# Kernel optimization log

Measured on AMD Instinct MI355X. Metric: run time of the kernel, lower is better.

## Reference

```python
import jax, jax.numpy as jnp
import numpy as np


def setup_inputs() -> dict:
    B, S, DK, DV, H = 2, 2048, 1024, 1024, 16
    ks = jax.random.split(jax.random.key(0), 7)
    keys = jax.random.normal(ks[0], (B, S, DK), jnp.float32)
    queries = jax.random.normal(ks[1], (B, S, DK), jnp.float32)
    values = jax.random.normal(ks[2], (B, S, DV), jnp.float32)
    # per-head projection weights, stored as [H, in, out] (torch Linear uses W.T; math-equivalent)
    WQ = jax.random.normal(ks[3], (H, DK, DK // H), jnp.float32) / np.sqrt(DK).astype(np.float32)
    WK = jax.random.normal(ks[4], (H, DK, DK // H), jnp.float32) / np.sqrt(DK).astype(np.float32)
    WV = jax.random.normal(ks[5], (H, DV, DV // H), jnp.float32) / np.sqrt(DV).astype(np.float32)
    WO = jax.random.normal(ks[6], (DV, DV), jnp.float32) / np.sqrt(DV).astype(np.float32)
    return {"keys": keys, "queries": queries, "values": values,
            "WQ": WQ, "WK": WK, "WV": WV, "WO": WO, "masking": 1}


def reference(keys, queries, values, WQ, WK, WV, WO, masking):
    B, Sq, _ = queries.shape
    Sk = keys.shape[1]
    # batched per-head projections (original loops over heads in Python)
    Q = jnp.einsum('bqd,hde->bhqe', queries, WQ)   # [B,H,Sq,dh]
    K = jnp.einsum('bkd,hde->bhke', keys, WK)      # [B,H,Sk,dh]
    V = jnp.einsum('bkd,hde->bhke', values, WV)    # [B,H,Sk,dvh]
    q_idx = jnp.arange(Sq)[:, None]
    k_idx = jnp.arange(Sk)[None, :]
    causal = k_idx <= q_idx
    # NOTE: original never applies the slope m; bias = (i - j) for i<=j else 0, same for all heads
    bias = jnp.where(causal, (k_idx - q_idx).astype(jnp.float32), 0.0)
    scale = np.float32(1.0 / np.sqrt(Sk))  # original divides by sqrt(keys.shape[1])
    y = (jnp.einsum('bhqe,bhke->bhqk', Q, K) + bias) * scale
    if masking:
        y = jnp.where(causal, y, -jnp.inf)
    # original: F.softmax(y, 1) on [B,Sq,Sk] -> softmax over the QUERY axis
    z = jax.nn.softmax(y, axis=2)
    out = jnp.einsum('bhqk,bhke->bhqe', z, V)      # [B,H,Sq,dvh]
    out = out.transpose(0, 2, 1, 3).reshape(B, Sq, -1)  # concat heads on last dim
    return out @ WO
```

## Files before the change

### kernel.cpp

```cpp
#include <hip/hip_runtime.h>
#include <math.h>

#define SEQ    2048
#define DMODEL 1024
#define NH     16
#define DH     64
#define NB     2
#define BHN    (NB*NH)

static constexpr float SCALE = 0.02209708691207961f;

typedef __attribute__((ext_vector_type(8))) short short8;
typedef __attribute__((ext_vector_type(4))) short short4v;
typedef __attribute__((ext_vector_type(4))) float f32x4;

__device__ __forceinline__ short f2bf(float f) {
    union { float f; unsigned u; } v; v.f = f;
    unsigned r = (v.u + 0x7FFFu + ((v.u >> 16) & 1u)) >> 16;
    return (short)r;
}

__device__ __forceinline__ unsigned pack_bf2(float a, float b) {
    union { float f; unsigned u; } ua, ub; ua.f = a; ub.f = b;
    return __builtin_amdgcn_perm(ub.u + 0x8000u, ua.u + 0x8000u, 0x07060302u);
}

__device__ __forceinline__ float bf2f(short s) {
    union { unsigned u; float f; } v; v.u = ((unsigned)(unsigned short)s) << 16;
    return v.f;
}

__device__ __forceinline__ void load16_lds(const short* g, short* l) {
    __builtin_amdgcn_global_load_lds(
        (const __attribute__((address_space(1))) unsigned int*)g,
        (__attribute__((address_space(3))) unsigned int*)l,
        16, 0, 0);
}

__device__ __forceinline__ void stage_rows(const short* g, short* s, int t, int ldg, int nIter) {
    int wave = t >> 6, lane = t & 63;
    #pragma unroll
    for (int i = 0; i < 4; ++i) {
        if (i >= nIter) break;
        int E   = i * 2048 + wave * 512 + lane * 8;
        int row = E >> 6;
        int blk = (lane & 7) ^ (row & 7);
        load16_lds(g + (size_t)row * ldg + blk * 8, s + i * 2048 + wave * 512);
    }
}

__device__ __forceinline__ short8 frag_sw(const short* s, int rowbase, int ks, int lane) {
    int m   = rowbase + (lane & 15);
    int q   = lane >> 4;
    int blk = (ks * 4 + q) ^ (m & 7);
    return *(const short8*)(s + m * 64 + blk * 8);
}

__global__ __launch_bounds__(256) void convert_all(
    const float* __restrict__ q, const float* __restrict__ k, const float* __restrict__ v,
    short* __restrict__ Xq, short* __restrict__ Xk, short* __restrict__ Xv,
    const float* __restrict__ WQ, const float* __restrict__ WK,
    const float* __restrict__ WV, const float* __restrict__ WO,
    short* __restrict__ WQt, short* __restrict__ WKt,
    short* __restrict__ WVt, short* __restrict__ WOt)
{
    __shared__ float Ts[64][68];
    const int lin = blockIdx.x;
    const int t = threadIdx.x;

    if (lin < 6144) {
        const int z = lin / 2048, bx = lin - z * 2048;
        const float* src = (z == 0) ? q : (z == 1) ? k : v;
        short* dst = (z == 0) ? Xq : (z == 1) ? Xk : Xv;
        size_t idx = ((size_t)bx * 256 + t) * 8;
        float4 a = *(const float4*)(src + idx);
        float4 b = *(const float4*)(src + idx + 4);
        short8 o;
        o[0] = f2bf(a.x); o[1] = f2bf(a.y); o[2] = f2bf(a.z); o[3] = f2bf(a.w);
        o[4] = f2bf(b.x); o[5] = f2bf(b.y); o[6] = f2bf(b.z); o[7] = f2bf(b.w);
        *(short8*)(dst + idx) = o;
        return;
    }

    const int wl = lin - 6144;
    const int z = wl >> 8, rem = wl & 255;
    const int k0 = (rem & 15) * 64;
    const int ny = rem >> 4;
    const float* W = (z == 0) ? WQ : (z == 1) ? WK : (z == 2) ? WV : WO;
    short* Wt = (z == 0) ? WQt : (z == 1) ? WKt : (z == 2) ? WVt : WOt;

    const int tr = t >> 4, tc4 = (t & 15) * 4;
    #pragma unroll
    for (int i = 0; i < 4; ++i) {
        int row = tr + i * 16;
        float4 v4;
        if (z < 3) v4 = *(const float4*)(W + (size_t)ny * DMODEL * DH + (size_t)(k0 + row) * DH + tc4);
        else       v4 = *(const float4*)(W + (size_t)(k0 + row) * DMODEL + ny * 64 + tc4);
        Ts[tc4 + 0][row] = v4.x; Ts[tc4 + 1][row] = v4.y;
        Ts[tc4 + 2][row] = v4.z; Ts[tc4 + 3][row] = v4.w;
    }
    __syncthreads();
    #pragma unroll
    for (int i = 0; i < 4; ++i) {
        int nl = tr + i * 16;
        short4v o;
        o[0] = f2bf(Ts[nl][tc4 + 0]); o[1] = f2bf(Ts[nl][tc4 + 1]);
        o[2] = f2bf(Ts[nl][tc4 + 2]); o[3] = f2bf(Ts[nl][tc4 + 3]);
        *(short4v*)(Wt + (size_t)(ny * 64 + nl) * DMODEL + k0 + tc4) = o;
    }
}

__global__ __launch_bounds__(256) void gemm_nt(
    const short* __restrict__ A0, const short* __restrict__ A1, const short* __restrict__ A2,
    const short* __restrict__ B0, const short* __restrict__ B1, const short* __restrict__ B2,
    short* __restrict__ Y0, short* __restrict__ Y1, short* __restrict__ Y2)
{
    const int z = blockIdx.z;
    const short* X  = (z == 0) ? A0 : (z == 1) ? A1 : A2;
    const short* Wt = (z == 0) ? B0 : (z == 1) ? B1 : B2;
    short* Y        = (z == 0) ? Y0 : (z == 1) ? Y1 : Y2;
    const bool vOrient = (z == 2);

    const int lin = blockIdx.y * 8 + blockIdx.x;
    const int n0 = (lin >> 5) * 128;
    const int m0 = (lin & 31) * 128;

    __shared__ short As[128 * 64];
    __shared__ short Bs[128 * 64];

    const int t = threadIdx.x;
    const int wave = t >> 6, lane = t & 63;
    const int wrow = (wave >> 1) * 64, wcol = (wave & 1) * 64;
    const int quad = lane >> 4, l15 = lane & 15;

    f32x4 acc[4][4];
    #pragma unroll
    for (int i = 0; i < 4; ++i)
        #pragma unroll
        for (int j = 0; j < 4; ++j)
            acc[i][j] = (f32x4)0.f;

    for (int k0 = 0; k0 < DMODEL; k0 += 64) {
        __syncthreads();
        stage_rows(X  + (size_t)m0 * DMODEL + k0, As, t, DMODEL, 4);
        stage_rows(Wt + (size_t)n0 * DMODEL + k0, Bs, t, DMODEL, 4);
        __syncthreads();
        if (!vOrient) {
            #pragma unroll
            for (int ks = 0; ks < 2; ++ks) {
                short8 xf[4], wf[4];
                #pragma unroll
                for (int i = 0; i < 4; ++i) xf[i] = frag_sw(As, wrow + i * 16, ks, lane);
                #pragma unroll
                for (int i = 0; i < 4; ++i) wf[i] = frag_sw(Bs, wcol + i * 16, ks, lane);
                #pragma unroll
                for (int a = 0; a < 4; ++a)
                    #pragma unroll
                    for (int b = 0; b < 4; ++b)
                        acc[a][b] = __builtin_amdgcn_mfma_f32_16x16x32_bf16(
                            wf[a], xf[b], acc[a][b], 0, 0, 0);
            }
        } else {
            #pragma unroll
            for (int ks = 0; ks < 2; ++ks) {
                short8 xf[4], wf[4];
                #pragma unroll
                for (int i = 0; i < 4; ++i) xf[i] = frag_sw(As, wrow + i * 16, ks, lane);
                #pragma unroll
                for (int i = 0; i < 4; ++i) wf[i] = frag_sw(Bs, wcol + i * 16, ks, lane);
                #pragma unroll
                for (int a = 0; a < 4; ++a)
                    #pragma unroll
                    for (int b = 0; b < 4; ++b)
                        acc[a][b] = __builtin_amdgcn_mfma_f32_16x16x32_bf16(
                            xf[a], wf[b], acc[a][b], 0, 0, 0);
            }
        }
    }

    if (vOrient) {
        #pragma unroll
        for (int a = 0; a < 4; ++a) {
            #pragma unroll
            for (int b = 0; b < 4; ++b) {
                int m = m0 + wrow + a * 16 + quad * 4;
                int n = n0 + wcol + b * 16 + l15;
                int bb = m >> 11, s = m & 2047, h = n >> 6, e = n & 63;
                short4v o;
                #pragma unroll
                for (int i = 0; i < 4; ++i) o[i] = f2bf(acc[a][b][i]);
                *(short4v*)(Y + ((size_t)((bb * NH + h) * DH + e)) * SEQ + s) = o;
            }
        }
    } else {
        #pragma unroll
        for (int a = 0; a < 4; ++a) {
            #pragma unroll
            for (int b = 0; b < 4; ++b) {
                int n = n0 + wcol + a * 16 + quad * 4;
                int m = m0 + wrow + b * 16 + l15;
                int bb = m >> 11, s = m & 2047, h = n >> 6, e = n & 63;
                short4v o;
                #pragma unroll
                for (int i = 0; i < 4; ++i) o[i] = f2bf(acc[a][b][i]);
                *(short4v*)(Y + ((size_t)((bb * NH + h) * SEQ + s)) * DH + e) = o;
            }
        }
    }
}

__global__ __launch_bounds__(256) void gemm_out(
    const short* __restrict__ X, const short* __restrict__ Wt,
    float* __restrict__ o0, float* __restrict__ o1)
{
    const int z = blockIdx.z;
    const int lin = blockIdx.y * 8 + blockIdx.x;
    const int n0 = (lin >> 5) * 128;
    const int m0 = (lin & 31) * 128;

    __shared__ short As[2][128 * 64];
    __shared__ short Bs[2][128 * 64];

    const int t = threadIdx.x;
    const int wave = t >> 6, lane = t & 63;
    const int wrow = (wave >> 1) * 64, wcol = (wave & 1) * 64;
    const int quad = lane >> 4, l15 = lane & 15;

    f32x4 acc[4][4];
    #pragma unroll
    for (int i = 0; i < 4; ++i)
        #pragma unroll
        for (int j = 0; j < 4; ++j)
            acc[i][j] = (f32x4)0.f;

    const int kBeg = z * 512;
    stage_rows(X  + (size_t)m0 * DMODEL + kBeg, As[0], t, DMODEL, 4);
    stage_rows(Wt + (size_t)n0 * DMODEL + kBeg, Bs[0], t, DMODEL, 4);
    __syncthreads();

    int cur = 0;
    for (int it = 0; it < 8; ++it) {
        if (it + 1 < 8) {
            const int k0 = kBeg + (it + 1) * 64;
            stage_rows(X  + (size_t)m0 * DMODEL + k0, As[cur ^ 1], t, DMODEL, 4);
            stage_rows(Wt + (size_t)n0 * DMODEL + k0, Bs[cur ^ 1], t, DMODEL, 4);
        }
        #pragma unroll
        for (int ks = 0; ks < 2; ++ks) {
            short8 xf[4], wf[4];
            #pragma unroll
            for (int i = 0; i < 4; ++i) xf[i] = frag_sw(As[cur], wrow + i * 16, ks, lane);
            #pragma unroll
            for (int i = 0; i < 4; ++i) wf[i] = frag_sw(Bs[cur], wcol + i * 16, ks, lane);
            #pragma unroll
            for (int a = 0; a < 4; ++a)
                #pragma unroll
                for (int b = 0; b < 4; ++b)
                    acc[a][b] = __builtin_amdgcn_mfma_f32_16x16x32_bf16(
                        wf[a], xf[b], acc[a][b], 0, 0, 0);
        }
        __syncthreads();
        cur ^= 1;
    }

    float* dst = z ? o1 : o0;
    #pragma unroll
    for (int a = 0; a < 4; ++a) {
        #pragma unroll
        for (int b = 0; b < 4; ++b) {
            int n = n0 + wcol + a * 16 + quad * 4;
            int m = m0 + wrow + b * 16 + l15;
            float4 o = make_float4(acc[a][b][0], acc[a][b][1], acc[a][b][2], acc[a][b][3]);
            *(float4*)(dst + (size_t)m * DMODEL + n) = o;
        }
    }
}

__global__ __launch_bounds__(256) void reduce_add(
    float* __restrict__ dst, const float* __restrict__ src)
{
    size_t i = ((size_t)blockIdx.x * 256 + threadIdx.x) * 8;
    float4 a0 = *(float4*)(dst + i);
    float4 a1 = *(float4*)(dst + i + 4);
    float4 b0 = *(const float4*)(src + i);
    float4 b1 = *(const float4*)(src + i + 4);
    a0.x += b0.x; a0.y += b0.y; a0.z += b0.z; a0.w += b0.w;
    a1.x += b1.x; a1.y += b1.y; a1.z += b1.z; a1.w += b1.w;
    *(float4*)(dst + i) = a0;
    *(float4*)(dst + i + 4) = a1;
}

__global__ __launch_bounds__(256) void stats_mfma(
    const short* __restrict__ Qg, const short* __restrict__ Kg,
    short* __restrict__ Vt, const int* __restrict__ mask_p)
{
    const int gblk = blockIdx.x;
    const int masking = mask_p[0];

    __shared__ short Ks[64 * 64];
    __shared__ short Qs[2][128 * 64];
    __shared__ float rsh[64];

    const int t = threadIdx.x;
    const int wave = t >> 6, lane = t & 63;
    const int quad = lane >> 4, l15 = lane & 15;

    for (int item = 0; item < 2; ++item) {
        const int w  = item ? (1023 - gblk) : gblk;
        const int kt = w >> 5, bh = w & 31;
        const int k0 = kt * 64;

        const int qb0 = masking ? (kt >> 1) : 0;
        const int q0s = qb0 * 128;
        if (item) __syncthreads();
        stage_rows(Kg + ((size_t)bh * SEQ + k0) * DH, Ks, t, DH, 2);
        stage_rows(Qg + ((size_t)bh * SEQ + q0s) * DH, Qs[0], t, DH, 4);
        __syncthreads();

        short8 Kf[2];
        Kf[0] = frag_sw(Ks, wave * 16, 0, lane);
        Kf[1] = frag_sw(Ks, wave * 16, 1, lane);

        int   kgi[4];
        float biasK[4];
        #pragma unroll
        for (int i = 0; i < 4; ++i) {
            kgi[i] = k0 + wave * 16 + quad * 4 + i;
            biasK[i] = SCALE * (float)kgi[i];
        }
        float qS[8];
        #pragma unroll
        for (int nt = 0; nt < 8; ++nt)
            qS[nt] = SCALE * (float)(q0s + nt * 16 + l15);

        float dsum[4] = {0.f, 0.f, 0.f, 0.f};
        const int nIter = masking ? (16 - qb0) : 16;
        for (int it = 0; it < nIter; ++it) {
            const int cur = it & 1;
            if (it > 0) __syncthreads();
            if (it + 1 < nIter)
                stage_rows(Qg + ((size_t)bh * SEQ + q0s + (it + 1) * 128) * DH, Qs[1 - cur], t, DH, 4);

            f32x4 acc[8];
            #pragma unroll
            for (int nt = 0; nt < 8; ++nt) acc[nt] = (f32x4)0.f;
            __builtin_amdgcn_s_setprio(1);
            #pragma unroll
            for (int ks = 0; ks < 2; ++ks)
                #pragma unroll
                for (int nt = 0; nt < 8; ++nt)
                    acc[nt] = __builtin_amdgcn_mfma_f32_16x16x32_bf16(
                        Kf[ks], frag_sw(Qs[cur], nt * 16, ks, lane), acc[nt], 0, 0, 0);
            __builtin_amdgcn_s_setprio(0);

            const bool exact = masking && (it == 0);
            #pragma unroll
            for (int nt = 0; nt < 8; ++nt) {
                #pragma unroll
                for (int i = 0; i < 4; ++i) {
                    float diff = biasK[i] - qS[nt];
                    float v = masking ? fmaf(acc[nt][i], SCALE, diff)
                                      : fmaf(acc[nt][i], SCALE, fminf(diff, 0.f));
                    float e = __expf(v);
                    if (exact)
                        e = (kgi[i] <= (q0s + nt * 16 + l15)) ? e : 0.f;
                    dsum[i] += e;
                }
            }
            #pragma unroll
            for (int nt = 0; nt < 8; ++nt) qS[nt] += 128.f * SCALE;
        }

        #pragma unroll
        for (int i = 0; i < 4; ++i) {
            float d = dsum[i];
            #pragma unroll
            for (int mm = 1; mm < 16; mm <<= 1) d += __shfl_xor(d, mm);
            dsum[i] = d;
        }
        if (l15 == 0) {
            #pragma unroll
            for (int i = 0; i < 4; ++i)
                rsh[wave * 16 + quad * 4 + i] = 1.f / dsum[i];
        }
        __syncthreads();

        short* Vs = Vt + (size_t)bh * DH * SEQ + k0;
        const int e  = t >> 2;
        const int sc = (t & 3) * 16;
        short8 v0 = *(short8*)(Vs + (size_t)e * SEQ + sc);
        short8 v1 = *(short8*)(Vs + (size_t)e * SEQ + sc + 8);
        union { unsigned u[4]; short8 s8; } o0, o1;
        #pragma unroll
        for (int j = 0; j < 4; ++j) {
            o0.u[j] = pack_bf2(bf2f(v0[2 * j])     * rsh[sc + 2 * j],
                               bf2f(v0[2 * j + 1]) * rsh[sc + 2 * j + 1]);
            o1.u[j] = pack_bf2(bf2f(v1[2 * j])     * rsh[sc + 8 + 2 * j],
                               bf2f(v1[2 * j + 1]) * rsh[sc + 8 + 2 * j + 1]);
        }
        *(short8*)(Vs + (size_t)e * SEQ + sc)     = o0.s8;
        *(short8*)(Vs + (size_t)e * SEQ + sc + 8) = o1.s8;
    }
}

template<int MODE>
__device__ __forceinline__ void attn_tile(
    const short* Kbuf, const short* Vbuf, short* Pw,
    const short8 Qf[2], const float bias[4][4], f32x4 oacc[4],
    int lane, int quad, int l15, int qloc)
{
    f32x4 sacc[4];
    #pragma unroll
    for (int mt = 0; mt < 4; ++mt) sacc[mt] = (f32x4)0.f;
    __builtin_amdgcn_s_setprio(1);
    #pragma unroll
    for (int ks = 0; ks < 2; ++ks) {
        #pragma unroll
        for (int mt = 0; mt < 4; ++mt)
            sacc[mt] = __builtin_amdgcn_mfma_f32_16x16x32_bf16(
                frag_sw(Kbuf, mt * 16, ks, lane), Qf[ks], sacc[mt], 0, 0, 0);
    }
    __builtin_amdgcn_s_setprio(0);
    __asm__ volatile("" ::: "memory");
    #pragma unroll
    for (int mt = 0; mt < 4; ++mt) {
        float p[4];
        #pragma unroll
        for (int i = 0; i < 4; ++i) {
            float bi = bias[mt][i];
            float v = (MODE == 2) ? fmaf(sacc[mt][i], SCALE, fminf(bi, 0.f))
                                  : fmaf(sacc[mt][i], SCALE, bi);
            float e = __expf(v);
            if (MODE == 1)
                e = ((mt * 16 + quad * 4 + i) <= qloc) ? e : 0.f;
            p[i] = e;
        }
        int blk = (2 * mt + (quad >> 1)) ^ (l15 & 7);
        *(uint2*)(Pw + l15 * 64 + blk * 8 + (quad & 1) * 4) =
            make_uint2(pack_bf2(p[0], p[1]), pack_bf2(p[2], p[3]));
    }
    __asm__ volatile("" ::: "memory");
    __builtin_amdgcn_s_setprio(1);
    #pragma unroll
    for (int ks = 0; ks < 2; ++ks) {
        short8 pf = *(const short8*)(Pw + l15 * 64 + (((ks * 4 + quad) ^ (l15 & 7)) * 8));
        #pragma unroll
        for (int mt = 0; mt < 4; ++mt)
            oacc[mt] = __builtin_amdgcn_mfma_f32_16x16x32_bf16(
                frag_sw(Vbuf, mt * 16, ks, lane), pf, oacc[mt], 0, 0, 0);
    }
    __builtin_amdgcn_s_setprio(0);
}

__global__ __launch_bounds__(256) void attn_mfma(
    const short* __restrict__ Qg, const short* __restrict__ Kg, const short* __restrict__ Vt,
    short* __restrict__ attnb, const int* __restrict__ mask_p)
{
    const int gblk = blockIdx.x;
    const int masking = mask_p[0];

    __shared__ short Qs[64 * 64];
    __shared__ short Ks[2][64 * 64];
    __shared__ short Vts[2][64 * 64];

    const int t = threadIdx.x;
    const int wave = t >> 6, lane = t & 63;
    const int quad = lane >> 4, l15 = lane & 15;
    short* Pw = Qs + wave * 1024;
    const int qloc = wave * 16 + l15;

    for (int item = 0; item < 2; ++item) {
        const int w  = item ? (1023 - gblk) : gblk;
        const int qt = w >> 5, bh = w & 31;
        const int b = bh >> 4, h = bh & (NH - 1);
        const int q0 = qt * 64;

        if (item) __syncthreads();
        stage_rows(Qg + ((size_t)bh * SEQ + q0) * DH, Qs, t, DH, 2);
        stage_rows(Kg + (size_t)bh * SEQ * DH, Ks[0], t, DH, 2);
        stage_rows(Vt + (size_t)bh * DH * SEQ, Vts[0], t, SEQ, 2);
        __syncthreads();

        short8 Qf[2];
        Qf[0] = frag_sw(Qs, wave * 16, 0, lane);
        Qf[1] = frag_sw(Qs, wave * 16, 1, lane);

        float bias[4][4];
        #pragma unroll
        for (int mt = 0; mt < 4; ++mt)
            #pragma unroll
            for (int i = 0; i < 4; ++i)
                bias[mt][i] = SCALE * (float)((mt * 16 + quad * 4 + i)
                                            - (q0 + qloc));

        f32x4 oacc[4];
        #pragma unroll
        for (int mt = 0; mt < 4; ++mt) oacc[mt] = (f32x4)0.f;

        const int nIter = masking ? (qt + 1) : (SEQ / 64);
        for (int it = 0; it < nIter; ++it) {
            const int cur = it & 1;
            if (it > 0) __syncthreads();
            if (it + 1 < nIter) {
                const int k0n = (it + 1) * 64;
                stage_rows(Kg + ((size_t)bh * SEQ + k0n) * DH, Ks[1 - cur], t, DH, 2);
                stage_rows(Vt + (size_t)bh * DH * SEQ + k0n, Vts[1 - cur], t, SEQ, 2);
            }
            if (!masking)       attn_tile<2>(Ks[cur], Vts[cur], Pw, Qf, bias, oacc, lane, quad, l15, qloc);
            else if (it == qt)  attn_tile<1>(Ks[cur], Vts[cur], Pw, Qf, bias, oacc, lane, quad, l15, qloc);
            else                attn_tile<0>(Ks[cur], Vts[cur], Pw, Qf, bias, oacc, lane, quad, l15, qloc);
            #pragma unroll
            for (int mt = 0; mt < 4; ++mt)
                #pragma unroll
                for (int i = 0; i < 4; ++i)
                    bias[mt][i] += 64.f * SCALE;
        }

        #pragma unroll
        for (int mt = 0; mt < 4; ++mt) {
            int e = mt * 16 + quad * 4;
            int q = q0 + wave * 16 + l15;
            short4v o;
            #pragma unroll
            for (int i = 0; i < 4; ++i) o[i] = f2bf(oacc[mt][i]);
            *(short4v*)(attnb + ((size_t)(b * SEQ + q)) * DMODEL + h * DH + e) = o;
        }
    }
}

extern "C" void kernel_launch(void* const* d_in, const int* in_sizes, int n_in,
                              void* d_out, int out_size, void* d_ws, size_t ws_size,
                              hipStream_t stream) {
    const float* keys    = (const float*)d_in[0];
    const float* queries = (const float*)d_in[1];
    const float* values  = (const float*)d_in[2];
    const float* WQ      = (const float*)d_in[3];
    const float* WK      = (const float*)d_in[4];
    const float* WV      = (const float*)d_in[5];
    const float* WO      = (const float*)d_in[6];
    const int*   mask_p  = (const int*)d_in[7];
    float* out = (float*)d_out;

    const size_t nX = (size_t)NB * SEQ * DMODEL;
    const size_t nW = (size_t)DMODEL * DMODEL;
    const size_t nQ = (size_t)BHN * SEQ * DH;

    short* ws = (short*)d_ws;
    short* Xq    = ws;
    short* Xk    = Xq + nX;
    short* Xv    = Xk + nX;
    short* WQt   = Xv + nX;
    short* WKt   = WQt + nW;
    short* WVt   = WKt + nW;
    short* WOt   = WVt + nW;
    short* Qg    = WOt + nW;
    short* Kg    = Qg + nQ;
    short* Vtg   = Kg + nQ;
    short* attnb = Vtg + nQ;
    float* outP1 = (float*)ws;

    convert_all<<<dim3(7168), dim3(256), 0, stream>>>(
        queries, keys, values, Xq, Xk, Xv,
        WQ, WK, WV, WO, WQt, WKt, WVt, WOt);
    gemm_nt<<<dim3(8, 32, 3), dim3(256), 0, stream>>>(
        Xq, Xk, Xv, WQt, WKt, WVt, Qg, Kg, Vtg);
    stats_mfma<<<dim3(512), dim3(256), 0, stream>>>(Qg, Kg, Vtg, mask_p);
    attn_mfma<<<dim3(512), dim3(256), 0, stream>>>(Qg, Kg, Vtg, attnb, mask_p);
    gemm_out<<<dim3(8, 32, 2), dim3(256), 0, stream>>>(attnb, WOt, out, outP1);
    reduce_add<<<dim3(2048), dim3(256), 0, stream>>>(out, outP1);
}
```

Measured before the change: 253.1 us.

## Drop split-K output GEMM and reduce pass; fold log2e into scale for exp2

The output projection no longer splits K into two halves written to separate buffers and summed by a reduce kernel. It now uses 128x64 tiles over the full K range across 512 blocks and writes the output directly, removing a launch and the extra fp32 read/write traffic. Separately, the softmax scale and bias are premultiplied by log2(e) so the exponential can use the hardware v_exp_f32 (exp2) instruction through inline asm instead of __expf. Each output-GEMM block now runs a longer K loop and reuses less of the B tile per block.

Result: faster. 239.3 us (-5.4%).

```diff
diff --git a/kernel.cpp b/kernel.cpp
--- a/kernel.cpp
+++ b/kernel.cpp
@@ -8,7 +8,8 @@
 #define NB     2
 #define BHN    (NB*NH)
 
-static constexpr float SCALE = 0.02209708691207961f;
+static constexpr float SCALE  = 0.02209708691207961f;
+static constexpr float SCALE2 = 0.02209708691207961f * 1.4426950408889634f;
 
 typedef __attribute__((ext_vector_type(8))) short short8;
 typedef __attribute__((ext_vector_type(4))) short short4v;
@@ -28,6 +29,12 @@
 __device__ __forceinline__ float bf2f(short s) {
     union { unsigned u; float f; } v; v.u = ((unsigned)(unsigned short)s) << 16;
     return v.f;
+}
+
+__device__ __forceinline__ float exp2_fast(float x) {
+    float r;
+    __asm__("v_exp_f32 %0, %1" : "=v"(r) : "v"(x));
+    return r;
 }
 
 __device__ __forceinline__ void load16_lds(const short* g, short* l) {
@@ -211,49 +218,47 @@
 
 __global__ __launch_bounds__(256) void gemm_out(
     const short* __restrict__ X, const short* __restrict__ Wt,
-    float* __restrict__ o0, float* __restrict__ o1)
+    float* __restrict__ outF)
 {
-    const int z = blockIdx.z;
-    const int lin = blockIdx.y * 8 + blockIdx.x;
-    const int n0 = (lin >> 5) * 128;
+    const int lin = blockIdx.x;
     const int m0 = (lin & 31) * 128;
+    const int n0 = (lin >> 5) * 64;
 
     __shared__ short As[2][128 * 64];
-    __shared__ short Bs[2][128 * 64];
+    __shared__ short Bs[2][64 * 64];
 
     const int t = threadIdx.x;
     const int wave = t >> 6, lane = t & 63;
-    const int wrow = (wave >> 1) * 64, wcol = (wave & 1) * 64;
+    const int wrow = (wave >> 1) * 64, wcol = (wave & 1) * 32;
     const int quad = lane >> 4, l15 = lane & 15;
 
-    f32x4 acc[4][4];
-    #pragma unroll
-    for (int i = 0; i < 4; ++i)
+    f32x4 acc[2][4];
+    #pragma unroll
+    for (int i = 0; i < 2; ++i)
         #pragma unroll
         for (int j = 0; j < 4; ++j)
             acc[i][j] = (f32x4)0.f;
 
-    const int kBeg = z * 512;
-    stage_rows(X  + (size_t)m0 * DMODEL + kBeg, As[0], t, DMODEL, 4);
-    stage_rows(Wt + (size_t)n0 * DMODEL + kBeg, Bs[0], t, DMODEL, 4);
+    stage_rows(X  + (size_t)m0 * DMODEL, As[0], t, DMODEL, 4);
+    stage_rows(Wt + (size_t)n0 * DMODEL, Bs[0], t, DMODEL, 2);
     __syncthreads();
 
     int cur = 0;
-    for (int it = 0; it < 8; ++it) {
-        if (it + 1 < 8) {
-            const int k0 = kBeg + (it + 1) * 64;
+    for (int it = 0; it < 16; ++it) {
+        if (it + 1 < 16) {
+            const int k0 = (it + 1) * 64;
             stage_rows(X  + (size_t)m0 * DMODEL + k0, As[cur ^ 1], t, DMODEL, 4);
-            stage_rows(Wt + (size_t)n0 * DMODEL + k0, Bs[cur ^ 1], t, DMODEL, 4);
+            stage_rows(Wt + (size_t)n0 * DMODEL + k0, Bs[cur ^ 1], t, DMODEL, 2);
         }
         #pragma unroll
         for (int ks = 0; ks < 2; ++ks) {
-            short8 xf[4], wf[4];
+            short8 xf[4], wf[2];
             #pragma unroll
             for (int i = 0; i < 4; ++i) xf[i] = frag_sw(As[cur], wrow + i * 16, ks, lane);
             #pragma unroll
-            for (int i = 0; i < 4; ++i) wf[i] = frag_sw(Bs[cur], wcol + i * 16, ks, lane);
-            #pragma unroll
-            for (int a = 0; a < 4; ++a)
+            for (int i = 0; i < 2; ++i) wf[i] = frag_sw(Bs[cur], wcol + i * 16, ks, lane);
+            #pragma unroll
+            for (int a = 0; a < 2; ++a)
                 #pragma unroll
                 for (int b = 0; b < 4; ++b)
                     acc[a][b] = __builtin_amdgcn_mfma_f32_16x16x32_bf16(
@@ -263,31 +268,16 @@
         cur ^= 1;
     }
 
-    float* dst = z ? o1 : o0;
-    #pragma unroll
-    for (int a = 0; a < 4; ++a) {
+    #pragma unroll
+    for (int a = 0; a < 2; ++a) {
         #pragma unroll
         for (int b = 0; b < 4; ++b) {
             int n = n0 + wcol + a * 16 + quad * 4;
             int m = m0 + wrow + b * 16 + l15;
             float4 o = make_float4(acc[a][b][0], acc[a][b][1], acc[a][b][2], acc[a][b][3]);
-            *(float4*)(dst + (size_t)m * DMODEL + n) = o;
-        }
-    }
-}
-
-__global__ __launch_bounds__(256) void reduce_add(
-    float* __restrict__ dst, const float* __restrict__ src)
-{
-    size_t i = ((size_t)blockIdx.x * 256 + threadIdx.x) * 8;
-    float4 a0 = *(float4*)(dst + i);
-    float4 a1 = *(float4*)(dst + i + 4);
-    float4 b0 = *(const float4*)(src + i);
-    float4 b1 = *(const float4*)(src + i + 4);
-    a0.x += b0.x; a0.y += b0.y; a0.z += b0.z; a0.w += b0.w;
-    a1.x += b1.x; a1.y += b1.y; a1.z += b1.z; a1.w += b1.w;
-    *(float4*)(dst + i) = a0;
-    *(float4*)(dst + i + 4) = a1;
+            *(float4*)(outF + (size_t)m * DMODEL + n) = o;
+        }
+    }
 }
 
 __global__ __launch_bounds__(256) void stats_mfma(
@@ -326,12 +316,12 @@
         #pragma unroll
         for (int i = 0; i < 4; ++i) {
             kgi[i] = k0 + wave * 16 + quad * 4 + i;
-            biasK[i] = SCALE * (float)kgi[i];
+            biasK[i] = SCALE2 * (float)kgi[i];
         }
         float qS[8];
         #pragma unroll
         for (int nt = 0; nt < 8; ++nt)
-            qS[nt] = SCALE * (float)(q0s + nt * 16 + l15);
+            qS[nt] = SCALE2 * (float)(q0s + nt * 16 + l15);
 
         float dsum[4] = {0.f, 0.f, 0.f, 0.f};
         const int nIter = masking ? (16 - qb0) : 16;
@@ -359,16 +349,16 @@
                 #pragma unroll
                 for (int i = 0; i < 4; ++i) {
                     float diff = biasK[i] - qS[nt];
-                    float v = masking ? fmaf(acc[nt][i], SCALE, diff)
-                                      : fmaf(acc[nt][i], SCALE, fminf(diff, 0.f));
-                    float e = __expf(v);
+                    float v = masking ? fmaf(acc[nt][i], SCALE2, diff)
+                                      : fmaf(acc[nt][i], SCALE2, fminf(diff, 0.f));
+                    float e = exp2_fast(v);
                     if (exact)
                         e = (kgi[i] <= (q0s + nt * 16 + l15)) ? e : 0.f;
                     dsum[i] += e;
                 }
             }
             #pragma unroll
-            for (int nt = 0; nt < 8; ++nt) qS[nt] += 128.f * SCALE;
+            for (int nt = 0; nt < 8; ++nt) qS[nt] += 128.f * SCALE2;
         }
 
         #pragma unroll
@@ -428,9 +418,9 @@
         #pragma unroll
         for (int i = 0; i < 4; ++i) {
             float bi = bias[mt][i];
-            float v = (MODE == 2) ? fmaf(sacc[mt][i], SCALE, fminf(bi, 0.f))
-                                  : fmaf(sacc[mt][i], SCALE, bi);
-            float e = __expf(v);
+            float v = (MODE == 2) ? fmaf(sacc[mt][i], SCALE2, fminf(bi, 0.f))
+                                  : fmaf(sacc[mt][i], SCALE2, bi);
+            float e = exp2_fast(v);
             if (MODE == 1)
                 e = ((mt * 16 + quad * 4 + i) <= qloc) ? e : 0.f;
             p[i] = e;
@@ -490,8 +480,8 @@
         for (int mt = 0; mt < 4; ++mt)
             #pragma unroll
             for (int i = 0; i < 4; ++i)
-                bias[mt][i] = SCALE * (float)((mt * 16 + quad * 4 + i)
-                                            - (q0 + qloc));
+                bias[mt][i] = SCALE2 * (float)((mt * 16 + quad * 4 + i)
+                                             - (q0 + qloc));
 
         f32x4 oacc[4];
         #pragma unroll
@@ -513,7 +503,7 @@
             for (int mt = 0; mt < 4; ++mt)
                 #pragma unroll
                 for (int i = 0; i < 4; ++i)
-                    bias[mt][i] += 64.f * SCALE;
+                    bias[mt][i] += 64.f * SCALE2;
         }
 
         #pragma unroll
@@ -557,7 +547,6 @@
     short* Kg    = Qg + nQ;
     short* Vtg   = Kg + nQ;
     short* attnb = Vtg + nQ;
-    float* outP1 = (float*)ws;
 
     convert_all<<<dim3(7168), dim3(256), 0, stream>>>(
         queries, keys, values, Xq, Xk, Xv,
@@ -566,6 +555,5 @@
         Xq, Xk, Xv, WQt, WKt, WVt, Qg, Kg, Vtg);
     stats_mfma<<<dim3(512), dim3(256), 0, stream>>>(Qg, Kg, Vtg, mask_p);
     attn_mfma<<<dim3(512), dim3(256), 0, stream>>>(Qg, Kg, Vtg, attnb, mask_p);
-    gemm_out<<<dim3(8, 32, 2), dim3(256), 0, stream>>>(attnb, WOt, out, outP1);
-    reduce_add<<<dim3(2048), dim3(256), 0, stream>>>(out, outP1);
-}
+    gemm_out<<<dim3(512), dim3(256), 0, stream>>>(attnb, WOt, out);
+}
```
